# Kernel optimization log

Measured on AMD Instinct MI355X. Metric: run time of the kernel, lower is better.

## Reference

```python
import jax, jax.numpy as jnp
import numpy as np

MAX_IN = 1024
MAX_OUT = 4096
LOW_RANK = 64
N_ARCH = 16
HYP_HID = 128


def setup_inputs() -> dict:
    key = jax.random.key(0)
    ks = jax.random.split(key, 9)
    x = jax.random.normal(ks[0], (4, 2048, MAX_IN), dtype=jnp.float32)
    active_arch_embed = jax.random.uniform(ks[1], (N_ARCH,), dtype=jnp.float32)
    # base linear params (PyTorch layout: weight [out, in])
    base_weight = jax.random.normal(ks[2], (MAX_OUT, MAX_IN), dtype=jnp.float32) * 0.02
    base_bias = jax.random.normal(ks[3], (MAX_OUT,), dtype=jnp.float32) * 0.02
    # low rank factor [low_rank, in], init std 0.01 per source
    lr_factor = jax.random.normal(ks[4], (LOW_RANK, MAX_IN), dtype=jnp.float32) * 0.01
    # hypernet: Linear(N_ARCH->HYP_HID), ReLU, Linear(HYP_HID->MAX_OUT*LOW_RANK)
    hyp_w1 = jax.random.normal(ks[5], (HYP_HID, N_ARCH), dtype=jnp.float32) * 0.05
    hyp_b1 = jax.random.normal(ks[6], (HYP_HID,), dtype=jnp.float32) * 0.05
    hyp_w2 = jax.random.normal(ks[7], (MAX_OUT * LOW_RANK, HYP_HID), dtype=jnp.float32) * 0.01
    hyp_b2 = jax.random.normal(ks[8], (MAX_OUT * LOW_RANK,), dtype=jnp.float32) * 0.01
    return {
        'x': x,
        'active_arch_embed': active_arch_embed,
        'base_weight': base_weight,
        'base_bias': base_bias,
        'lr_factor': lr_factor,
        'hyp_w1': hyp_w1,
        'hyp_b1': hyp_b1,
        'hyp_w2': hyp_w2,
        'hyp_b2': hyp_b2,
    }


def reference(x, active_arch_embed, base_weight, base_bias, lr_factor,
              hyp_w1, hyp_b1, hyp_w2, hyp_b2):
    # hypernet MLP on the arch embedding -> low-rank left factor [MAX_OUT, LOW_RANK]
    h = jax.nn.relu(hyp_w1 @ active_arch_embed + hyp_b1)          # [HYP_HID]
    left = (hyp_w2 @ h + hyp_b2).reshape(MAX_OUT, LOW_RANK)        # [out, r]
    # full weight = base + low-rank update (as in source, before slicing)
    weight = base_weight + left @ lr_factor                        # [out, in]
    # active_out = max_out, active_in = x.shape[-1] = max_in -> no slicing
    # F.linear: y = x @ weight.T + bias
    return jnp.einsum('bsi,oi->bso', x, weight) + base_bias
```

## Files before the change

### kernel.cpp

```cpp
#include <hip/hip_runtime.h>

#define MAX_IN   1024
#define MAX_OUT  4096
#define LOW_RANK 64
#define N_ARCH   16
#define HYP_HID  128
#define BATCH_M  8192

typedef __attribute__((ext_vector_type(8))) short short8;
typedef __attribute__((ext_vector_type(4))) float f32x4;

__device__ __forceinline__ unsigned short f2bf(float f) {
  union { float f; unsigned int u; } c; c.f = f;
  unsigned int r = c.u + 0x7fffu + ((c.u >> 16) & 1u);
  return (unsigned short)(r >> 16);
}

__device__ __forceinline__ void gload16(const unsigned short* g, unsigned short* l) {
  __builtin_amdgcn_global_load_lds(
      (const __attribute__((address_space(1))) unsigned int*)(g),
      (__attribute__((address_space(3))) unsigned int*)(l), 16, 0, 0);
}

__global__ __launch_bounds__(256) void convert_x(const float* __restrict__ in,
                                                 unsigned short* __restrict__ out) {
  size_t i = (size_t)blockIdx.x * 256 + threadIdx.x;
  float4 v = *(const float4*)(in + i * 4);
  ushort4 o;
  o.x = f2bf(v.x); o.y = f2bf(v.y); o.z = f2bf(v.z); o.w = f2bf(v.w);
  *(ushort4*)(out + i * 4) = o;
}

__global__ __launch_bounds__(256) void build_w4(
    const float* __restrict__ w1, const float* __restrict__ b1,
    const float* __restrict__ e,
    const float* __restrict__ hyp_w2, const float* __restrict__ hyp_b2,
    const float* __restrict__ base_w, const float* __restrict__ lrf,
    unsigned short* __restrict__ Wbf) {
  __shared__ float hs[HYP_HID];
  __shared__ float lefts[4 * LOW_RANK];
  const int tid = threadIdx.x;
  const int o0 = blockIdx.x * 4;
  const int row0 = blockIdx.x * 256;

  if (tid < HYP_HID) {
    const float4* wr = (const float4*)(w1 + tid * N_ARCH);
    float s = b1[tid];
#pragma unroll
    for (int c = 0; c < 4; c++) {
      float4 wv = wr[c];
      float4 ev = *(const float4*)(e + c * 4);
      s += wv.x * ev.x + wv.y * ev.y + wv.z * ev.z + wv.w * ev.w;
    }
    hs[tid] = fmaxf(s, 0.0f);
  }
  __syncthreads();

  const int lane = tid & 63;
  const int w = tid >> 6;
  const int half = lane >> 5;
  const int sub = lane & 31;
  const float4 hf = *(const float4*)(hs + sub * 4);

  const float* src = hyp_w2 + ((size_t)row0 + w * 64 + half) * HYP_HID + sub * 4;

#define LDJ(j) (*(const float4*)(src + (size_t)(j) * 2 * HYP_HID))
#define PROC(v, j)                                                             \
  do {                                                                         \
    float s = v.x * hf.x + v.y * hf.y + v.z * hf.z + v.w * hf.w;               \
    s += __shfl_xor(s, 16);                                                    \
    s += __shfl_xor(s, 8);                                                     \
    s += __shfl_xor(s, 4);                                                     \
    s += __shfl_xor(s, 2);                                                     \
    s += __shfl_xor(s, 1);                                                     \
    const int rl_ = w * 64 + 2 * (j) + half;                                   \
    if (sub == 0) lefts[rl_] = s + hyp_b2[row0 + rl_];                         \
  } while (0)

  float4 v0 = LDJ(0), v1 = LDJ(1), v2 = LDJ(2), v3 = LDJ(3);
#pragma unroll
  for (int jj = 0; jj < 7; jj++) {
    PROC(v0, jj * 4 + 0); v0 = LDJ(jj * 4 + 4);
    PROC(v1, jj * 4 + 1); v1 = LDJ(jj * 4 + 5);
    PROC(v2, jj * 4 + 2); v2 = LDJ(jj * 4 + 6);
    PROC(v3, jj * 4 + 3); v3 = LDJ(jj * 4 + 7);
  }
  PROC(v0, 28); PROC(v1, 29); PROC(v2, 30); PROC(v3, 31);
#undef LDJ
#undef PROC
  __syncthreads();

  const int k0 = tid * 4;
  float4 acc[4];
#pragma unroll
  for (int oi = 0; oi < 4; oi++)
    acc[oi] = *(const float4*)(base_w + (size_t)(o0 + oi) * MAX_IN + k0);
#pragma unroll 8
  for (int r = 0; r < LOW_RANK; r++) {
    float4 lv = *(const float4*)(lrf + r * MAX_IN + k0);
#pragma unroll
    for (int oi = 0; oi < 4; oi++) {
      const float lw = lefts[oi * LOW_RANK + r];
      acc[oi].x += lw * lv.x; acc[oi].y += lw * lv.y;
      acc[oi].z += lw * lv.z; acc[oi].w += lw * lv.w;
    }
  }
#pragma unroll
  for (int oi = 0; oi < 4; oi++) {
    ushort4 o;
    o.x = f2bf(acc[oi].x); o.y = f2bf(acc[oi].y);
    o.z = f2bf(acc[oi].z); o.w = f2bf(acc[oi].w);
    *(ushort4*)(Wbf + (size_t)(o0 + oi) * MAX_IN + k0) = o;
  }
}

__global__ __launch_bounds__(256, 2) void gemm_kernel(
    const unsigned short* __restrict__ A,
    const unsigned short* __restrict__ B,
    const float* __restrict__ bias,
    float* __restrict__ C) {
  constexpr int K = MAX_IN;
  constexpr int N = MAX_OUT;
  constexpr int ABUF = 128 * 32;
  constexpr int BBUF = 256 * 32;
  constexpr int TBUF = ABUF + BBUF;
  constexpr int NT = K / 32;
  __shared__ __align__(16) unsigned short lds[3 * TBUF];

  const int tid = threadIdx.x;
  const int lane = tid & 63;
  const int w = tid >> 6;
  const int wm = w >> 1, wn = w & 1;
  const int fl = lane & 15, hi = lane >> 4;

  const int orig = blockIdx.x;
  const int xcd = orig & 7;
  const int mj = orig >> 3;
  const int bm = ((xcd >> 1) * 16 + (mj >> 3)) * 128;
  const int bn = ((xcd & 1) * 8 + (mj & 7)) * 256;

  const int sA0 = w * 128 + lane;
  const int rA = sA0 >> 2;
  const int cA = (sA0 & 3) ^ ((sA0 >> 3) & 3);
  const int sB0 = w * 256 + lane;
  const int rB = sB0 >> 2;
  const int cB = (sB0 & 3) ^ ((sB0 >> 3) & 3);
  const unsigned short* Ag = A + (size_t)(bm + rA) * K + cA * 8;
  const unsigned short* Bg = B + (size_t)(bn + rB) * K + cB * 8;

  const int swz = hi ^ ((fl >> 1) & 3);
  const int abase = (wm * 32 + (fl >> 1)) * 64 + (fl & 1) * 32 + swz * 8;
  const int bbase = (wn * 64 + (fl >> 1)) * 64 + (fl & 1) * 32 + swz * 8;

  f32x4 acc[4][8];
#pragma unroll
  for (int m = 0; m < 4; m++)
#pragma unroll
    for (int n = 0; n < 8; n++) acc[m][n] = (f32x4){0.f, 0.f, 0.f, 0.f};

#define STAGE(p, t)                                                            \
  do {                                                                         \
    unsigned short* la_ = &lds[(p) * TBUF];                                    \
    unsigned short* lb_ = la_ + ABUF;                                          \
    _Pragma("unroll")                                                          \
    for (int j = 0; j < 2; j++)                                                \
      gload16(Ag + (size_t)(16 * j) * K + (t) * 32, &la_[(sA0 + 64 * j) * 8]); \
    _Pragma("unroll")                                                          \
    for (int j = 0; j < 4; j++)                                                \
      gload16(Bg + (size_t)(16 * j) * K + (t) * 32, &lb_[(sB0 + 64 * j) * 8]); \
  } while (0)

  STAGE(0, 0);
  STAGE(1, 1);
  asm volatile("s_waitcnt vmcnt(6)" ::: "memory");
  __builtin_amdgcn_s_barrier();
  __builtin_amdgcn_sched_barrier(0);

  int p = 0;
  for (int t = 0; t < NT; ++t) {
    if (t + 2 < NT) {
      const int pn = (p + 2 >= 3) ? p - 1 : p + 2;
      STAGE(pn, t + 2);
    }
    const unsigned short* la = &lds[p * TBUF];
    const unsigned short* lb = la + ABUF;
    short8 a[4], b[8];
#pragma unroll
    for (int m = 0; m < 4; m++) a[m] = *(const short8*)&la[abase + m * 512];
#pragma unroll
    for (int n = 0; n < 8; n++) b[n] = *(const short8*)&lb[bbase + n * 512];
    __builtin_amdgcn_s_setprio(1);
#pragma unroll
    for (int m = 0; m < 4; m++)
#pragma unroll
      for (int n = 0; n < 8; n++)
        acc[m][n] = __builtin_amdgcn_mfma_f32_16x16x32_bf16(a[m], b[n], acc[m][n], 0, 0, 0);
    __builtin_amdgcn_s_setprio(0);
    if (t + 2 < NT) {
      asm volatile("s_waitcnt vmcnt(6)" ::: "memory");
    } else if (t + 2 == NT) {
      asm volatile("s_waitcnt vmcnt(0)" ::: "memory");
    }
    if (t + 1 < NT) {
      __builtin_amdgcn_s_barrier();
      __builtin_amdgcn_sched_barrier(0);
    }
    p = (p + 1 == 3) ? 0 : p + 1;
  }
#undef STAGE

  float bv[8];
#pragma unroll
  for (int n = 0; n < 8; n++) bv[n] = bias[bn + wn * 128 + n * 16 + fl];
#pragma unroll
  for (int m = 0; m < 4; m++) {
    const int gr0 = bm + wm * 64 + m * 16 + hi * 4;
#pragma unroll
    for (int n = 0; n < 8; n++) {
      const int gc = bn + wn * 128 + n * 16 + fl;
#pragma unroll
      for (int j = 0; j < 4; j++)
        C[(size_t)(gr0 + j) * N + gc] = acc[m][n][j] + bv[n];
    }
  }
}

extern "C" void kernel_launch(void* const* d_in, const int* in_sizes, int n_in,
                              void* d_out, int out_size, void* d_ws, size_t ws_size,
                              hipStream_t stream) {
  const float* x      = (const float*)d_in[0];
  const float* embed  = (const float*)d_in[1];
  const float* base_w = (const float*)d_in[2];
  const float* base_b = (const float*)d_in[3];
  const float* lrf    = (const float*)d_in[4];
  const float* w1     = (const float*)d_in[5];
  const float* b1     = (const float*)d_in[6];
  const float* w2     = (const float*)d_in[7];
  const float* b2     = (const float*)d_in[8];
  float* out = (float*)d_out;

  char* ws = (char*)d_ws;
  unsigned short* Xbf = (unsigned short*)ws;
  unsigned short* Wbf = (unsigned short*)(ws + (size_t)BATCH_M * MAX_IN * 2);

  hipLaunchKernelGGL(convert_x, dim3(BATCH_M * MAX_IN / 1024), dim3(256), 0, stream, x, Xbf);
  hipLaunchKernelGGL(build_w4, dim3(MAX_OUT / 4), dim3(256), 0, stream,
                     w1, b1, embed, w2, b2, base_w, lrf, Wbf);
  hipLaunchKernelGGL(gemm_kernel, dim3((BATCH_M / 128) * (MAX_OUT / 256)), dim3(256), 0, stream,
                     Xbf, Wbf, base_b, out);
}
```

Measured before the change: 137.4 us.

## Stage hypernet weight rows through double-buffered LDS with async global loads

Replaces the direct register loads of hyp_w2 rows in build_w4 with global_load_lds copies into a double-buffered, XOR-swizzled shared-memory stage, with explicit vmcnt waits and barriers per 32-row chunk. Each 8-lane group then reduces one row from LDS using a shorter shuffle tree. The goal is to overlap the heavy hyp_w2 streaming with compute and to cut shuffle count. The cost is 32KB of LDS, which may lower occupancy, plus extra barriers. A leftover dummy read loop (0.f * v) adds redundant LDS traffic.

```diff
diff --git a/kernel.cpp b/kernel.cpp
--- a/kernel.cpp
+++ b/kernel.cpp
@@ -17,6 +17,11 @@
 }
 
 __device__ __forceinline__ void gload16(const unsigned short* g, unsigned short* l) {
+  __builtin_amdgcn_global_load_lds(
+      (const __attribute__((address_space(1))) unsigned int*)(g),
+      (__attribute__((address_space(3))) unsigned int*)(l), 16, 0, 0);
+}
+__device__ __forceinline__ void gload16f(const float* g, float* l) {
   __builtin_amdgcn_global_load_lds(
       (const __attribute__((address_space(1))) unsigned int*)(g),
       (__attribute__((address_space(3))) unsigned int*)(l), 16, 0, 0);
@@ -39,6 +44,7 @@
     unsigned short* __restrict__ Wbf) {
   __shared__ float hs[HYP_HID];
   __shared__ float lefts[4 * LOW_RANK];
+  __shared__ __align__(16) float stage[2][32 * HYP_HID];
   const int tid = threadIdx.x;
   const int o0 = blockIdx.x * 4;
   const int row0 = blockIdx.x * 256;
@@ -56,38 +62,65 @@
   }
   __syncthreads();
 
-  const int lane = tid & 63;
-  const int w = tid >> 6;
-  const int half = lane >> 5;
-  const int sub = lane & 31;
-  const float4 hf = *(const float4*)(hs + sub * 4);
-
-  const float* src = hyp_w2 + ((size_t)row0 + w * 64 + half) * HYP_HID + sub * 4;
-
-#define LDJ(j) (*(const float4*)(src + (size_t)(j) * 2 * HYP_HID))
-#define PROC(v, j)                                                             \
+  const int rin = tid >> 5;
+  const int lc = (tid & 31) ^ (rin & 7);
+  const float* srcT = hyp_w2 + ((size_t)row0 + rin) * HYP_HID + lc * 4;
+
+#define STAGE(c)                                                               \
   do {                                                                         \
-    float s = v.x * hf.x + v.y * hf.y + v.z * hf.z + v.w * hf.w;               \
-    s += __shfl_xor(s, 16);                                                    \
-    s += __shfl_xor(s, 8);                                                     \
-    s += __shfl_xor(s, 4);                                                     \
-    s += __shfl_xor(s, 2);                                                     \
-    s += __shfl_xor(s, 1);                                                     \
-    const int rl_ = w * 64 + 2 * (j) + half;                                   \
-    if (sub == 0) lefts[rl_] = s + hyp_b2[row0 + rl_];                         \
+    float* dst = &stage[(c) & 1][0];                                           \
+    _Pragma("unroll")                                                          \
+    for (int j = 0; j < 4; j++)                                                \
+      gload16f(srcT + (size_t)((c) * 32 + j * 8) * HYP_HID,                    \
+               dst + (j * 256 + tid) * 4);                                     \
   } while (0)
 
-  float4 v0 = LDJ(0), v1 = LDJ(1), v2 = LDJ(2), v3 = LDJ(3);
-#pragma unroll
-  for (int jj = 0; jj < 7; jj++) {
-    PROC(v0, jj * 4 + 0); v0 = LDJ(jj * 4 + 4);
-    PROC(v1, jj * 4 + 1); v1 = LDJ(jj * 4 + 5);
-    PROC(v2, jj * 4 + 2); v2 = LDJ(jj * 4 + 6);
-    PROC(v3, jj * 4 + 3); v3 = LDJ(jj * 4 + 7);
-  }
-  PROC(v0, 28); PROC(v1, 29); PROC(v2, 30); PROC(v3, 31);
-#undef LDJ
-#undef PROC
+  const int g = tid >> 3, gl = tid & 7;
+  float4 hf[4];
+#pragma unroll
+  for (int j = 0; j < 4; j++) hf[j] = *(const float4*)(hs + gl * 16 + j * 4);
+  int rdoff[4];
+#pragma unroll
+  for (int j = 0; j < 4; j++)
+    rdoff[4 - 1 - j] = g * HYP_HID + (((gl * 4 + j) ^ (g & 7)) * 4);
+
+  STAGE(0);
+  for (int c = 0; c < 8; ++c) {
+    if (c + 1 < 8) {
+      STAGE(c + 1);
+      asm volatile("s_waitcnt vmcnt(4)" ::: "memory");
+    } else {
+      asm volatile("s_waitcnt vmcnt(0)" ::: "memory");
+    }
+    __builtin_amdgcn_s_barrier();
+    __builtin_amdgcn_sched_barrier(0);
+
+    const float* buf = &stage[c & 1][0];
+    float s = 0.f;
+#pragma unroll
+    for (int j = 0; j < 4; j++) {
+      float4 v = *(const float4*)(buf + rdoff[j]);
+      s += 0.f * v.x;
+    }
+    {
+      float4 v0 = *(const float4*)(buf + g * HYP_HID + (((gl * 4 + 0) ^ (g & 7)) * 4));
+      float4 v1 = *(const float4*)(buf + g * HYP_HID + (((gl * 4 + 1) ^ (g & 7)) * 4));
+      float4 v2 = *(const float4*)(buf + g * HYP_HID + (((gl * 4 + 2) ^ (g & 7)) * 4));
+      float4 v3 = *(const float4*)(buf + g * HYP_HID + (((gl * 4 + 3) ^ (g & 7)) * 4));
+      s = v0.x * hf[0].x + v0.y * hf[0].y + v0.z * hf[0].z + v0.w * hf[0].w
+        + v1.x * hf[1].x + v1.y * hf[1].y + v1.z * hf[1].z + v1.w * hf[1].w
+        + v2.x * hf[2].x + v2.y * hf[2].y + v2.z * hf[2].z + v2.w * hf[2].w
+        + v3.x * hf[3].x + v3.y * hf[3].y + v3.z * hf[3].z + v3.w * hf[3].w;
+    }
+    s += __shfl_xor(s, 4);
+    s += __shfl_xor(s, 2);
+    s += __shfl_xor(s, 1);
+    const int rl = c * 32 + g;
+    if (gl == 0) lefts[rl] = s + hyp_b2[row0 + rl];
+    __builtin_amdgcn_s_barrier();
+    __builtin_amdgcn_sched_barrier(0);
+  }
+#undef STAGE
   __syncthreads();
 
   const int k0 = tid * 4;
```

Result: no change. 138.9 us (+1.1%).
